# Kernel optimization log

Measured on AMD Instinct MI355X. Metric: run time of the kernel, lower is better.

## Reference

```python
import jax, jax.numpy as jnp
import numpy as np

B, T, C, NH, DH, L, HFF, FEAT = 2, 1024, 1024, 16, 64, 4, 2816, 9
EPS = 1e-5
ROPE_BASE = 10000.0


def setup_inputs() -> dict:
    key = jax.random.key(0)
    ks = jax.random.split(key, 11)
    s = 0.02
    return {
        "x": jax.random.normal(ks[0], (B, T, FEAT), jnp.float32),
        "w_in": jax.random.normal(ks[1], (C, FEAT), jnp.float32) * s,
        "wq": jax.random.normal(ks[2], (L, C, C), jnp.float32) * s,
        "wkv": jax.random.normal(ks[3], (L, 2 * C, C), jnp.float32) * s,
        "wo": jax.random.normal(ks[4], (L, C, C), jnp.float32) * s,
        "w1": jax.random.normal(ks[5], (L, HFF, C), jnp.float32) * s,
        "w2": jax.random.normal(ks[6], (L, HFF, C), jnp.float32) * s,
        "w3": jax.random.normal(ks[7], (L, C, HFF), jnp.float32) * s,
        "g1": jnp.ones((L, C), jnp.float32),
        "g2": jnp.ones((L, C), jnp.float32),
        "gf": jnp.ones((C,), jnp.float32),
    }


def _rms(x, g):
    # lag-llama RMSNorm: x * rsqrt(mean(x^2) + eps) * scale
    return x * jax.lax.rsqrt(jnp.mean(x * x, axis=-1, keepdims=True) + EPS) * g


def _rope_tables(seq_len, dim):
    inv_freq = 1.0 / (ROPE_BASE ** (jnp.arange(0, dim, 2, dtype=jnp.float32) / dim))
    freqs = jnp.arange(seq_len, dtype=jnp.float32)[:, None] * inv_freq[None, :]
    emb = jnp.concatenate([freqs, freqs], axis=-1)  # [T, DH]
    return jnp.cos(emb), jnp.sin(emb)


def _rotate_half(x):
    h = x.shape[-1] // 2
    return jnp.concatenate([-x[..., h:], x[..., :h]], axis=-1)


def reference(x, w_in, wq, wkv, wo, w1, w2, w3, g1, g2, gf):
    h = x @ w_in.T  # [B,T,C] input projection (wte)
    cos, sin = _rope_tables(T, DH)  # [T,DH], broadcast over B,NH
    causal = jnp.tril(jnp.ones((T, T), dtype=bool))
    scale = 1.0 / np.sqrt(DH).astype(np.float32)

    for l in range(L):
        # --- attention block ---
        a_in = _rms(h, g1[l])
        q = (a_in @ wq[l].T).reshape(B, T, NH, DH).transpose(0, 2, 1, 3)
        kv = a_in @ wkv[l].T
        k = kv[..., :C].reshape(B, T, NH, DH).transpose(0, 2, 1, 3)
        v = kv[..., C:].reshape(B, T, NH, DH).transpose(0, 2, 1, 3)
        q = q * cos + _rotate_half(q) * sin
        k = k * cos + _rotate_half(k) * sin
        scores = jnp.einsum('bhtd,bhsd->bhts', q, k) * scale
        scores = jnp.where(causal, scores, -jnp.inf)
        probs = jax.nn.softmax(scores, axis=-1)  # dropout_p=0 -> identity
        y = jnp.einsum('bhts,bhsd->bhtd', probs, v)
        y = y.transpose(0, 2, 1, 3).reshape(B, T, C)
        h = h + y @ wo[l].T
        # --- MLP block (gated SiLU) ---
        m_in = _rms(h, g2[l])
        h = h + (jax.nn.silu(m_in @ w1[l].T) * (m_in @ w2[l].T)) @ w3[l].T

    return _rms(h, gf)
```

## Files before the change

kernel.cpp:

```cpp
#include <hip/hip_runtime.h>
#include <hip/hip_bf16.h>


#define B_   2
#define T_   1024
#define C_   1024
#define NH_  16
#define DH_  64
#define L_   4
#define HFF_ 2816
#define EPS_ 1e-5f

typedef unsigned short u16;
typedef short bf16x8 __attribute__((ext_vector_type(8)));
typedef float f32x4 __attribute__((ext_vector_type(4)));

__device__ __forceinline__ float b2f(u16 u) {
    union { unsigned int i; float f; } v; v.i = ((unsigned int)u) << 16; return v.f;
}
__device__ __forceinline__ u16 f2b(float f) {
    union { unsigned int i; float f; } v; v.f = f;
    unsigned int r = (v.i + 0x7fff + ((v.i >> 16) & 1)) >> 16;
    return (u16)r;
}

__global__ void detect_k(const unsigned int* __restrict__ xw, int* __restrict__ flag)
{
    int tid = threadIdx.x;
    int cnt = 0;
#pragma unroll
    for (int i = 0; i < 4; ++i) {
        unsigned int w = xw[tid * 4 + i];
        unsigned int e = (w >> 7) & 0xFF;
        if (e >= 0x70 && e <= 0x87) cnt++;
    }
#pragma unroll
    for (int off = 32; off; off >>= 1) cnt += __shfl_down(cnt, off);
    if (tid == 0) flag[0] = (cnt > 128) ? 0 : 1;
}

__global__ void cvt_k(const void* __restrict__ src, u16* __restrict__ dst,
                      int n, const int* __restrict__ flag)
{
    int f = flag[0];
    int i = blockIdx.x * 256 + threadIdx.x;
    int stride = gridDim.x * 256;
    if (f) {
        const float* s = (const float*)src;
        for (; i < n; i += stride) dst[i] = f2b(s[i]);
    } else {
        const u16* s = (const u16*)src;
        for (; i < n; i += stride) dst[i] = s[i];
    }
}

template<int MODE>
__global__ __launch_bounds__(256, 2)
void gemm_bt(const u16* __restrict__ A, const u16* __restrict__ Bm,
             u16* __restrict__ Cb, float* __restrict__ Cf,
             int M, int N, int K, int lda, int ldb, int ldc,
             int nhDiv, long sAb, long sAh, long sBb, long sBh,
             long sCb, long sCh)
{
    __shared__ __align__(16) u16 tA[128 * 32];
    __shared__ __align__(16) u16 tB[128 * 32];

    const int z  = blockIdx.z;
    const int bb = z / nhDiv;
    const int hh = z - bb * nhDiv;
    const u16* Ab = A + bb * sAb + hh * sAh;
    const u16* Bb = Bm + bb * sBb + hh * sBh;
    const long cOff = bb * sCb + hh * sCh;

    const int row0 = blockIdx.y * 128;
    const int col0 = blockIdx.x * 128;
    const int tid  = threadIdx.x;
    const int lane = tid & 63;
    const int wave = tid >> 6;
    const int wr = wave >> 1, wc = wave & 1;
    const int lrow = lane & 15;
    const int kg   = lane >> 4;

    int r_[2], cg_[2];
#pragma unroll
    for (int i = 0; i < 2; ++i) {
        int chunk = i * 256 + tid;
        r_[i]  = chunk >> 2;
        cg_[i] = chunk & 3;
    }

    f32x4 acc[4][4] = {};

    for (int k0 = 0; k0 < K; k0 += 32) {
        bf16x8 ra[2], rb[2];
#pragma unroll
        for (int i = 0; i < 2; ++i) {
            const u16* ga = Ab + (long)(row0 + r_[i]) * lda + (k0 + cg_[i] * 8);
            ra[i] = *(const bf16x8*)ga;
            int rB = col0 + r_[i]; if (rB > N - 1) rB = N - 1;
            const u16* gb = Bb + (long)rB * ldb + (k0 + cg_[i] * 8);
            rb[i] = *(const bf16x8*)gb;
        }
        __syncthreads();
#pragma unroll
        for (int i = 0; i < 2; ++i) {
            int chunk = i * 256 + tid;
            *(bf16x8*)&tA[(size_t)chunk * 8] = ra[i];
            *(bf16x8*)&tB[(size_t)chunk * 8] = rb[i];
        }
        __syncthreads();

        bf16x8 af[4], bfr[4];
#pragma unroll
        for (int ti = 0; ti < 4; ++ti)
            af[ti] = *(const bf16x8*)&tA[(wr * 64 + ti * 16 + lrow) * 32 + kg * 8];
#pragma unroll
        for (int tj = 0; tj < 4; ++tj)
            bfr[tj] = *(const bf16x8*)&tB[(wc * 64 + tj * 16 + lrow) * 32 + kg * 8];
#pragma unroll
        for (int ti = 0; ti < 4; ++ti)
#pragma unroll
            for (int tj = 0; tj < 4; ++tj)
                acc[ti][tj] = __builtin_amdgcn_mfma_f32_16x16x32_bf16(
                    af[ti], bfr[tj], acc[ti][tj], 0, 0, 0);
    }

    const int rbase = row0 + wr * 64;
    const int cbase = col0 + wc * 64 + lrow;
#pragma unroll
    for (int ti = 0; ti < 4; ++ti) {
#pragma unroll
        for (int r = 0; r < 4; ++r) {
            int row = rbase + ti * 16 + kg * 4 + r;
#pragma unroll
            for (int tj = 0; tj < 4; ++tj) {
                int col = cbase + tj * 16;
                if (col < N) {
                    long off = cOff + (long)row * ldc + col;
                    if (MODE == 0) Cb[off] = f2b(acc[ti][tj][r]);
                    else           Cf[off] += acc[ti][tj][r];
                }
            }
        }
    }
}

__global__ void input_proj_k(const u16* __restrict__ x, const u16* __restrict__ w,
                             float* __restrict__ h)
{
    int idx = blockIdx.x * 256 + threadIdx.x;
    int bt = idx >> 10, c = idx & 1023;
    float s = 0.f;
#pragma unroll
    for (int f = 0; f < 9; ++f) s += b2f(x[bt * 9 + f]) * b2f(w[c * 9 + f]);
    h[idx] = s;
}

__global__ void rms_k(const float* __restrict__ h, const u16* __restrict__ g,
                      void* __restrict__ out, int isFinal,
                      const int* __restrict__ flag)
{
    __shared__ float red[8];
    const int row = blockIdx.x;
    const float* hr = h + (size_t)row * C_;
    float ss = 0.f;
    for (int c = threadIdx.x; c < C_; c += 256) { float v = hr[c]; ss += v * v; }
#pragma unroll
    for (int off = 32; off; off >>= 1) ss += __shfl_down(ss, off);
    int lane = threadIdx.x & 63, wave = threadIdx.x >> 6;
    if (lane == 0) red[wave] = ss;
    __syncthreads();
    if (threadIdx.x == 0)
        red[4] = rsqrtf((red[0] + red[1] + red[2] + red[3]) / (float)C_ + EPS_);
    __syncthreads();
    float r = red[4];
    const int f32out = isFinal && flag[0];
    for (int c = threadIdx.x; c < C_; c += 256) {
        float val = hr[c] * r * b2f(g[c]);
        size_t o = (size_t)row * C_ + c;
        if (f32out) ((float*)out)[o] = val;
        else        ((u16*)out)[o]   = f2b(val);
    }
}

__global__ void rope_k(u16* __restrict__ q, u16* __restrict__ kv)
{
    int idx = blockIdx.x * 256 + threadIdx.x;
    int i = idx & 31;
    int hh = (idx >> 5) & 15;
    int t = (idx >> 9) & 1023;
    int b = idx >> 19;
    float invf = powf(10000.0f, -(float)i / 32.0f);
    float fr = (float)t * invf;
    float cf = cosf(fr), sf = sinf(fr);

    size_t qo = ((size_t)(b * 1024 + t) << 10) + hh * 64 + i;
    float x1 = b2f(q[qo]), x2 = b2f(q[qo + 32]);
    q[qo]      = f2b(x1 * cf - x2 * sf);
    q[qo + 32] = f2b(x2 * cf + x1 * sf);

    size_t ko = ((size_t)(b * 1024 + t) << 11) + hh * 64 + i;
    x1 = b2f(kv[ko]); x2 = b2f(kv[ko + 32]);
    kv[ko]      = f2b(x1 * cf - x2 * sf);
    kv[ko + 32] = f2b(x2 * cf + x1 * sf);
}

__global__ void vtrans_k(const u16* __restrict__ kv, u16* __restrict__ vt)
{
    int idx = blockIdx.x * 256 + threadIdx.x;
    int s = idx & 1023;
    int d = (idx >> 10) & 63;
    int hh = (idx >> 16) & 15;
    int b = idx >> 20;
    vt[idx] = kv[((size_t)(b * 1024 + s) << 11) + 1024 + hh * 64 + d];
}

__global__ void softmax_k(u16* __restrict__ S)
{
    __shared__ float red[8];
    const int t = blockIdx.x & 1023;
    const int z = blockIdx.x >> 10;
    u16* row = S + ((size_t)z << 20) + ((size_t)t << 10);
    const int n = t + 1;
    const int tid = threadIdx.x;
    const int lane = tid & 63, wave = tid >> 6;

    float mx = -1e30f;
    for (int c = tid; c < n; c += 256) mx = fmaxf(mx, 0.125f * b2f(row[c]));
#pragma unroll
    for (int off = 32; off; off >>= 1) mx = fmaxf(mx, __shfl_down(mx, off));
    if (lane == 0) red[wave] = mx;
    __syncthreads();
    if (tid == 0) red[4] = fmaxf(fmaxf(red[0], red[1]), fmaxf(red[2], red[3]));
    __syncthreads();
    const float M = red[4];

    float sum = 0.f;
    for (int c = tid; c < n; c += 256) sum += __expf(0.125f * b2f(row[c]) - M);
#pragma unroll
    for (int off = 32; off; off >>= 1) sum += __shfl_down(sum, off);
    if (lane == 0) red[wave] = sum;
    __syncthreads();
    if (tid == 0) red[5] = red[0] + red[1] + red[2] + red[3];
    __syncthreads();
    const float inv = 1.0f / red[5];

    for (int c = tid; c < 1024; c += 256) {
        float p = (c < n) ? __expf(0.125f * b2f(row[c]) - M) * inv : 0.f;
        row[c] = f2b(p);
    }
}

__global__ void silu_mul_k(u16* __restrict__ u1, const u16* __restrict__ u2)
{
    size_t idx = (size_t)blockIdx.x * 256 + threadIdx.x;
    float a = b2f(u1[idx]);
    float m = a / (1.f + __expf(-a));
    u1[idx] = f2b(m * b2f(u2[idx]));
}

static inline void launch_gemm(bool add, const u16* A, const u16* Bm, void* C,
                               int M, int N, int K, int lda, int ldb, int ldc,
                               int batch, int nhDiv,
                               long sAb, long sAh, long sBb, long sBh,
                               long sCb, long sCh, hipStream_t stream)
{
    dim3 g((N + 127) / 128, M / 128, batch);
    if (add)
        gemm_bt<1><<<g, 256, 0, stream>>>(A, Bm, nullptr, (float*)C,
            M, N, K, lda, ldb, ldc, nhDiv, sAb, sAh, sBb, sBh, sCb, sCh);
    else
        gemm_bt<0><<<g, 256, 0, stream>>>(A, Bm, (u16*)C, nullptr,
            M, N, K, lda, ldb, ldc, nhDiv, sAb, sAh, sBb, sBh, sCb, sCh);
}

extern "C" void kernel_launch(void* const* d_in, const int* in_sizes, int n_in,
                              void* d_out, int out_size, void* d_ws, size_t ws_size,
                              hipStream_t stream)
{
    char* w = (char*)d_ws;
    float* h  = (float*)w;
    u16* a    = (u16*)(w + (8u  << 20));
    u16* q    = (u16*)(w + (12u << 20));
    u16* kv   = (u16*)(w + (16u << 20));
    u16* vt   = (u16*)(w + (24u << 20));
    u16* y    = (u16*)(w + (28u << 20));
    u16* S    = (u16*)(w + (32u << 20));
    u16* u1   = S;
    u16* u2   = S + (size_t)2048 * HFF_;

    size_t off = (size_t)64 << 20;
    const int nelem[11] = {
        B_ * T_ * 9,
        C_ * 9,
        L_ * C_ * C_,
        L_ * 2 * C_ * C_,
        L_ * C_ * C_,
        L_ * HFF_ * C_,
        L_ * HFF_ * C_,
        L_ * C_ * HFF_,
        L_ * C_,
        L_ * C_,
        C_
    };
    u16* cbuf[11];
    for (int i = 0; i < 11; ++i) {
        cbuf[i] = (u16*)(w + off);
        off += ((size_t)nelem[i] * 2 + 255) & ~(size_t)255;
    }
    int* flag = (int*)(w + off);

    detect_k<<<1, 64, 0, stream>>>((const unsigned int*)d_in[0], flag);
    for (int i = 0; i < 11; ++i) {
        int blocks = (nelem[i] + 255) / 256; if (blocks > 2048) blocks = 2048;
        cvt_k<<<blocks, 256, 0, stream>>>(d_in[i], cbuf[i], nelem[i], flag);
    }
    const u16* cx   = cbuf[0];
    const u16* cwin = cbuf[1];
    const u16* cwq  = cbuf[2];
    const u16* cwkv = cbuf[3];
    const u16* cwo  = cbuf[4];
    const u16* cw1  = cbuf[5];
    const u16* cw2  = cbuf[6];
    const u16* cw3  = cbuf[7];
    const u16* cg1  = cbuf[8];
    const u16* cg2  = cbuf[9];
    const u16* cgf  = cbuf[10];

    const long TC  = (long)T_ * C_;
    const long T2C = 2 * TC;
    const long TT  = (long)T_ * T_;

    input_proj_k<<<8192, 256, 0, stream>>>(cx, cwin, h);

    for (int l = 0; l < L_; ++l) {
        const u16* wq_l  = cwq  + (size_t)l * C_ * C_;
        const u16* wkv_l = cwkv + (size_t)l * 2 * C_ * C_;
        const u16* wo_l  = cwo  + (size_t)l * C_ * C_;
        const u16* w1_l  = cw1  + (size_t)l * HFF_ * C_;
        const u16* w2_l  = cw2  + (size_t)l * HFF_ * C_;
        const u16* w3_l  = cw3  + (size_t)l * C_ * HFF_;

        rms_k<<<2048, 256, 0, stream>>>(h, cg1 + l * C_, a, 0, flag);
        launch_gemm(false, a, wq_l, q, 2048, 1024, 1024, 1024, 1024, 1024,
                    1, 1, 0, 0, 0, 0, 0, 0, stream);
        launch_gemm(false, a, wkv_l, kv, 2048, 2048, 1024, 1024, 1024, 2048,
                    1, 1, 0, 0, 0, 0, 0, 0, stream);
        rope_k<<<4096, 256, 0, stream>>>(q, kv);
        vtrans_k<<<8192, 256, 0, stream>>>(kv, vt);

        for (int b = 0; b < B_; ++b) {
            const u16* qb  = q  + (size_t)b * TC;
            const u16* kvb = kv + (size_t)b * T2C;
            const u16* vtb = vt + (size_t)b * NH_ * DH_ * T_;
            u16* yb        = y  + (size_t)b * TC;
            launch_gemm(false, qb, kvb, S, 1024, 1024, 64, 1024, 2048, 1024,
                        16, 16, 0, 64, 0, 64, 0, TT, stream);
            softmax_k<<<16 * 1024, 256, 0, stream>>>(S);
            launch_gemm(false, S, vtb, yb, 1024, 64, 1024, 1024, 1024, 1024,
                        16, 16, 0, TT, 0, (long)DH_ * T_, 0, DH_, stream);
        }
        launch_gemm(true, y, wo_l, h, 2048, 1024, 1024, 1024, 1024, 1024,
                    1, 1, 0, 0, 0, 0, 0, 0, stream);

        rms_k<<<2048, 256, 0, stream>>>(h, cg2 + l * C_, a, 0, flag);
        launch_gemm(false, a, w1_l, u1, 2048, HFF_, 1024, 1024, 1024, HFF_,
                    1, 1, 0, 0, 0, 0, 0, 0, stream);
        launch_gemm(false, a, w2_l, u2, 2048, HFF_, 1024, 1024, 1024, HFF_,
                    1, 1, 0, 0, 0, 0, 0, 0, stream);
        silu_mul_k<<<22528, 256, 0, stream>>>(u1, u2);
        launch_gemm(true, u1, w3_l, h, 2048, 1024, HFF_, HFF_, HFF_, 1024,
                    1, 1, 0, 0, 0, 0, 0, 0, stream);
    }

    rms_k<<<2048, 256, 0, stream>>>(h, cgf, d_out, 1, flag);
}
```

Before: 1.786 ms.

## Fuse QKV and W1/W2 GEMMs, split-K residual GEMMs, load tiles directly to LDS

Weights are repacked at conversion time so Q/K/V and W1/W2 each sit in one buffer, and each pair or triple is computed by a single batched GEMM launch. The residual-add GEMMs (wo, w3) are split four ways along K and accumulate into h with atomicAdd, so the 16x8 tile grid covers more of the CUs. The GEMM tile loads now use global_load_lds, copying straight from global memory into LDS instead of going through registers. The conversion kernel is vectorized to four elements per thread. In exchange, float atomics make the summation order nondeterministic, and the direct-to-LDS loads depend on the compiler inserting the correct wait before the barrier.

```diff
diff --git a/kernel.cpp b/kernel.cpp
--- a/kernel.cpp
+++ b/kernel.cpp
@@ -40,17 +40,24 @@
 }
 
 __global__ void cvt_k(const void* __restrict__ src, u16* __restrict__ dst,
-                      int n, const int* __restrict__ flag)
-{
-    int f = flag[0];
-    int i = blockIdx.x * 256 + threadIdx.x;
-    int stride = gridDim.x * 256;
-    if (f) {
-        const float* s = (const float*)src;
-        for (; i < n; i += stride) dst[i] = f2b(s[i]);
-    } else {
-        const u16* s = (const u16*)src;
-        for (; i < n; i += stride) dst[i] = s[i];
+                      long perV, long dstStrideV, long dstOffV,
+                      const int* __restrict__ flag)
+{
+    const int f = flag[0];
+    long y = blockIdx.y;
+    long i = (long)blockIdx.x * 256 + threadIdx.x;
+    long stride = (long)gridDim.x * 256;
+    for (; i < perV; i += stride) {
+        long so = y * perV + i;
+        long dj = y * dstStrideV + dstOffV + i;
+        ushort4 o;
+        if (f) {
+            float4 v = ((const float4*)src)[so];
+            o.x = f2b(v.x); o.y = f2b(v.y); o.z = f2b(v.z); o.w = f2b(v.w);
+        } else {
+            o = ((const ushort4*)src)[so];
+        }
+        ((ushort4*)dst)[dj] = o;
     }
 }
 
@@ -60,17 +67,26 @@
              u16* __restrict__ Cb, float* __restrict__ Cf,
              int M, int N, int K, int lda, int ldb, int ldc,
              int nhDiv, long sAb, long sAh, long sBb, long sBh,
-             long sCb, long sCh)
+             long sCb, long sCh, int kSplit)
 {
     __shared__ __align__(16) u16 tA[128 * 32];
     __shared__ __align__(16) u16 tB[128 * 32];
 
-    const int z  = blockIdx.z;
-    const int bb = z / nhDiv;
-    const int hh = z - bb * nhDiv;
-    const u16* Ab = A + bb * sAb + hh * sAh;
-    const u16* Bb = Bm + bb * sBb + hh * sBh;
-    const long cOff = bb * sCb + hh * sCh;
+    const int z = blockIdx.z;
+    int kBeg = 0, kEnd = K;
+    const u16* Ab = A;
+    const u16* Bb = Bm;
+    long cOff = 0;
+    if (MODE == 1) {
+        int ks = K / kSplit;
+        kBeg = z * ks; kEnd = kBeg + ks;
+    } else {
+        int bb = z / nhDiv;
+        int hh = z - bb * nhDiv;
+        Ab += bb * sAb + hh * sAh;
+        Bb += bb * sBb + hh * sBh;
+        cOff = bb * sCb + hh * sCh;
+    }
 
     const int row0 = blockIdx.y * 128;
     const int col0 = blockIdx.x * 128;
@@ -81,32 +97,30 @@
     const int lrow = lane & 15;
     const int kg   = lane >> 4;
 
-    int r_[2], cg_[2];
-#pragma unroll
-    for (int i = 0; i < 2; ++i) {
-        int chunk = i * 256 + tid;
-        r_[i]  = chunk >> 2;
-        cg_[i] = chunk & 3;
-    }
-
     f32x4 acc[4][4] = {};
 
-    for (int k0 = 0; k0 < K; k0 += 32) {
-        bf16x8 ra[2], rb[2];
-#pragma unroll
-        for (int i = 0; i < 2; ++i) {
-            const u16* ga = Ab + (long)(row0 + r_[i]) * lda + (k0 + cg_[i] * 8);
-            ra[i] = *(const bf16x8*)ga;
-            int rB = col0 + r_[i]; if (rB > N - 1) rB = N - 1;
-            const u16* gb = Bb + (long)rB * ldb + (k0 + cg_[i] * 8);
-            rb[i] = *(const bf16x8*)gb;
-        }
+    for (int k0 = kBeg; k0 < kEnd; k0 += 32) {
         __syncthreads();
 #pragma unroll
         for (int i = 0; i < 2; ++i) {
             int chunk = i * 256 + tid;
-            *(bf16x8*)&tA[(size_t)chunk * 8] = ra[i];
-            *(bf16x8*)&tB[(size_t)chunk * 8] = rb[i];
+            int r = chunk >> 2, cg = chunk & 3;
+            const u16* ga = Ab + (long)(row0 + r) * lda + (k0 + cg * 8);
+            u16* la = tA + (size_t)(i * 256 + wave * 64) * 8;
+            __builtin_amdgcn_global_load_lds(
+                (const __attribute__((address_space(1))) void*)ga,
+                (__attribute__((address_space(3))) void*)la, 16, 0, 0);
+        }
+#pragma unroll
+        for (int i = 0; i < 2; ++i) {
+            int chunk = i * 256 + tid;
+            int r = chunk >> 2, cg = chunk & 3;
+            int rB = col0 + r; if (rB > N - 1) rB = N - 1;
+            const u16* gb = Bb + (long)rB * ldb + (k0 + cg * 8);
+            u16* lb = tB + (size_t)(i * 256 + wave * 64) * 8;
+            __builtin_amdgcn_global_load_lds(
+                (const __attribute__((address_space(1))) void*)gb,
+                (__attribute__((address_space(3))) void*)lb, 16, 0, 0);
         }
         __syncthreads();
 
@@ -138,7 +152,7 @@
                 if (col < N) {
                     long off = cOff + (long)row * ldc + col;
                     if (MODE == 0) Cb[off] = f2b(acc[ti][tj][r]);
-                    else           Cf[off] += acc[ti][tj][r];
+                    else           atomicAdd(&Cf[off], acc[ti][tj][r]);
                 }
             }
         }
@@ -183,7 +197,7 @@
     }
 }
 
-__global__ void rope_k(u16* __restrict__ q, u16* __restrict__ kv)
+__global__ void rope_k(u16* __restrict__ qkv)
 {
     int idx = blockIdx.x * 256 + threadIdx.x;
     int i = idx & 31;
@@ -194,25 +208,25 @@
     float fr = (float)t * invf;
     float cf = cosf(fr), sf = sinf(fr);
 
-    size_t qo = ((size_t)(b * 1024 + t) << 10) + hh * 64 + i;
-    float x1 = b2f(q[qo]), x2 = b2f(q[qo + 32]);
-    q[qo]      = f2b(x1 * cf - x2 * sf);
-    q[qo + 32] = f2b(x2 * cf + x1 * sf);
-
-    size_t ko = ((size_t)(b * 1024 + t) << 11) + hh * 64 + i;
-    x1 = b2f(kv[ko]); x2 = b2f(kv[ko + 32]);
-    kv[ko]      = f2b(x1 * cf - x2 * sf);
-    kv[ko + 32] = f2b(x2 * cf + x1 * sf);
-}
-
-__global__ void vtrans_k(const u16* __restrict__ kv, u16* __restrict__ vt)
+    size_t base = (size_t)(b * 1024 + t) * 3072 + hh * 64 + i;
+    float x1 = b2f(qkv[base]), x2 = b2f(qkv[base + 32]);
+    qkv[base]      = f2b(x1 * cf - x2 * sf);
+    qkv[base + 32] = f2b(x2 * cf + x1 * sf);
+
+    size_t kb = base + 1024;
+    x1 = b2f(qkv[kb]); x2 = b2f(qkv[kb + 32]);
+    qkv[kb]      = f2b(x1 * cf - x2 * sf);
+    qkv[kb + 32] = f2b(x2 * cf + x1 * sf);
+}
+
+__global__ void vtrans_k(const u16* __restrict__ qkv, u16* __restrict__ vt)
 {
     int idx = blockIdx.x * 256 + threadIdx.x;
     int s = idx & 1023;
     int d = (idx >> 10) & 63;
     int hh = (idx >> 16) & 15;
     int b = idx >> 20;
-    vt[idx] = kv[((size_t)(b * 1024 + s) << 11) + 1024 + hh * 64 + d];
+    vt[idx] = qkv[(size_t)(b * 1024 + s) * 3072 + 2048 + hh * 64 + d];
 }
 
 __global__ void softmax_k(u16* __restrict__ S)
@@ -261,17 +275,26 @@
 
 static inline void launch_gemm(bool add, const u16* A, const u16* Bm, void* C,
                                int M, int N, int K, int lda, int ldb, int ldc,
-                               int batch, int nhDiv,
+                               int zdim, int nhDiv,
                                long sAb, long sAh, long sBb, long sBh,
-                               long sCb, long sCh, hipStream_t stream)
-{
-    dim3 g((N + 127) / 128, M / 128, batch);
+                               long sCb, long sCh, int kSplit, hipStream_t stream)
+{
+    dim3 g((N + 127) / 128, M / 128, zdim);
     if (add)
         gemm_bt<1><<<g, 256, 0, stream>>>(A, Bm, nullptr, (float*)C,
-            M, N, K, lda, ldb, ldc, nhDiv, sAb, sAh, sBb, sBh, sCb, sCh);
+            M, N, K, lda, ldb, ldc, nhDiv, sAb, sAh, sBb, sBh, sCb, sCh, kSplit);
     else
         gemm_bt<0><<<g, 256, 0, stream>>>(A, Bm, (u16*)C, nullptr,
-            M, N, K, lda, ldb, ldc, nhDiv, sAb, sAh, sBb, sBh, sCb, sCh);
+            M, N, K, lda, ldb, ldc, nhDiv, sAb, sAh, sBb, sBh, sCb, sCh, kSplit);
+}
+
+static inline void launch_cvt(const void* src, u16* dst, long perV,
+                              long dstStrideV, long dstOffV, int chunks,
+                              const int* flag, hipStream_t stream)
+{
+    long bx = (perV + 255) / 256; if (bx > 512) bx = 512;
+    dim3 g((unsigned)bx, (unsigned)chunks, 1);
+    cvt_k<<<g, 256, 0, stream>>>(src, dst, perV, dstStrideV, dstOffV, flag);
 }
 
 extern "C" void kernel_launch(void* const* d_in, const int* in_sizes, int n_in,
@@ -279,98 +302,81 @@
                               hipStream_t stream)
 {
     char* w = (char*)d_ws;
-    float* h  = (float*)w;
-    u16* a    = (u16*)(w + (8u  << 20));
-    u16* q    = (u16*)(w + (12u << 20));
-    u16* kv   = (u16*)(w + (16u << 20));
-    u16* vt   = (u16*)(w + (24u << 20));
-    u16* y    = (u16*)(w + (28u << 20));
-    u16* S    = (u16*)(w + (32u << 20));
-    u16* u1   = S;
-    u16* u2   = S + (size_t)2048 * HFF_;
+    float* h   = (float*)w;
+    u16* a     = (u16*)(w + (8u  << 20));
+    u16* qkv   = (u16*)(w + (12u << 20));
+    u16* vt    = (u16*)(w + (24u << 20));
+    u16* y     = (u16*)(w + (28u << 20));
+    u16* S     = (u16*)(w + (32u << 20));
+    u16* u1    = S;
+    u16* u2    = S + (size_t)2048 * HFF_;
 
     size_t off = (size_t)64 << 20;
-    const int nelem[11] = {
-        B_ * T_ * 9,
-        C_ * 9,
-        L_ * C_ * C_,
-        L_ * 2 * C_ * C_,
-        L_ * C_ * C_,
-        L_ * HFF_ * C_,
-        L_ * HFF_ * C_,
-        L_ * C_ * HFF_,
-        L_ * C_,
-        L_ * C_,
-        C_
-    };
-    u16* cbuf[11];
-    for (int i = 0; i < 11; ++i) {
-        cbuf[i] = (u16*)(w + off);
-        off += ((size_t)nelem[i] * 2 + 255) & ~(size_t)255;
-    }
-    int* flag = (int*)(w + off);
+    u16* cx    = (u16*)(w + off); off += ((size_t)B_*T_*9*2   + 255) & ~(size_t)255;
+    u16* cwin  = (u16*)(w + off); off += ((size_t)C_*9*2      + 255) & ~(size_t)255;
+    u16* cwqkv = (u16*)(w + off); off += (size_t)L_*3072*1024*2;
+    u16* cwo   = (u16*)(w + off); off += (size_t)L_*C_*C_*2;
+    u16* cw12  = (u16*)(w + off); off += (size_t)L_*2*HFF_*C_*2;
+    u16* cw3   = (u16*)(w + off); off += (size_t)L_*C_*HFF_*2;
+    u16* cg1   = (u16*)(w + off); off += ((size_t)L_*C_*2 + 255) & ~(size_t)255;
+    u16* cg2   = (u16*)(w + off); off += ((size_t)L_*C_*2 + 255) & ~(size_t)255;
+    u16* cgf   = (u16*)(w + off); off += ((size_t)C_*2    + 255) & ~(size_t)255;
+    int* flag  = (int*)(w + off);
 
     detect_k<<<1, 64, 0, stream>>>((const unsigned int*)d_in[0], flag);
-    for (int i = 0; i < 11; ++i) {
-        int blocks = (nelem[i] + 255) / 256; if (blocks > 2048) blocks = 2048;
-        cvt_k<<<blocks, 256, 0, stream>>>(d_in[i], cbuf[i], nelem[i], flag);
-    }
-    const u16* cx   = cbuf[0];
-    const u16* cwin = cbuf[1];
-    const u16* cwq  = cbuf[2];
-    const u16* cwkv = cbuf[3];
-    const u16* cwo  = cbuf[4];
-    const u16* cw1  = cbuf[5];
-    const u16* cw2  = cbuf[6];
-    const u16* cw3  = cbuf[7];
-    const u16* cg1  = cbuf[8];
-    const u16* cg2  = cbuf[9];
-    const u16* cgf  = cbuf[10];
+
+    const long CCv  = (long)C_ * C_ / 4;
+    const long HCv  = (long)HFF_ * C_ / 4;
+    launch_cvt(d_in[0],  cx,    (long)B_*T_*9/4, 0, 0, 1, flag, stream);
+    launch_cvt(d_in[1],  cwin,  (long)C_*9/4,    0, 0, 1, flag, stream);
+    launch_cvt(d_in[2],  cwqkv, CCv,   3*CCv, 0,     L_, flag, stream);
+    launch_cvt(d_in[3],  cwqkv, 2*CCv, 3*CCv, CCv,   L_, flag, stream);
+    launch_cvt(d_in[4],  cwo,   CCv,   CCv,   0,     L_, flag, stream);
+    launch_cvt(d_in[5],  cw12,  HCv,   2*HCv, 0,     L_, flag, stream);
+    launch_cvt(d_in[6],  cw12,  HCv,   2*HCv, HCv,   L_, flag, stream);
+    launch_cvt(d_in[7],  cw3,   HCv,   HCv,   0,     L_, flag, stream);
+    launch_cvt(d_in[8],  cg1,   (long)L_*C_/4, 0, 0, 1, flag, stream);
+    launch_cvt(d_in[9],  cg2,   (long)L_*C_/4, 0, 0, 1, flag, stream);
+    launch_cvt(d_in[10], cgf,   (long)C_/4,    0, 0, 1, flag, stream);
 
     const long TC  = (long)T_ * C_;
-    const long T2C = 2 * TC;
     const long TT  = (long)T_ * T_;
+    const long TQ  = (long)T_ * 3072;
 
     input_proj_k<<<8192, 256, 0, stream>>>(cx, cwin, h);
 
     for (int l = 0; l < L_; ++l) {
-        const u16* wq_l  = cwq  + (size_t)l * C_ * C_;
-        const u16* wkv_l = cwkv + (size_t)l * 2 * C_ * C_;
-        const u16* wo_l  = cwo  + (size_t)l * C_ * C_;
-        const u16* w1_l  = cw1  + (size_t)l * HFF_ * C_;
-        const u16* w2_l  = cw2  + (size_t)l * HFF_ * C_;
-        const u16* w3_l  = cw3  + (size_t)l * C_ * HFF_;
+        const u16* wqkv_l = cwqkv + (size_t)l * 3072 * 1024;
+        const u16* wo_l   = cwo   + (size_t)l * C_ * C_;
+        const u16* w12_l  = cw12  + (size_t)l * 2 * HFF_ * C_;
+        const u16* w3_l   = cw3   + (size_t)l * C_ * HFF_;
 
         rms_k<<<2048, 256, 0, stream>>>(h, cg1 + l * C_, a, 0, flag);
-        launch_gemm(false, a, wq_l, q, 2048, 1024, 1024, 1024, 1024, 1024,
-                    1, 1, 0, 0, 0, 0, 0, 0, stream);
-        launch_gemm(false, a, wkv_l, kv, 2048, 2048, 1024, 1024, 1024, 2048,
-                    1, 1, 0, 0, 0, 0, 0, 0, stream);
-        rope_k<<<4096, 256, 0, stream>>>(q, kv);
-        vtrans_k<<<8192, 256, 0, stream>>>(kv, vt);
+        launch_gemm(false, a, wqkv_l, qkv, 2048, 1024, 1024, 1024, 1024, 3072,
+                    3, 3, 0, 0, 0, (long)C_*C_, 0, 1024, 1, stream);
+        rope_k<<<4096, 256, 0, stream>>>(qkv);
+        vtrans_k<<<8192, 256, 0, stream>>>(qkv, vt);
 
         for (int b = 0; b < B_; ++b) {
-            const u16* qb  = q  + (size_t)b * TC;
-            const u16* kvb = kv + (size_t)b * T2C;
+            const u16* qb = qkv + (size_t)b * TQ;
+            const u16* kb = qb + 1024;
             const u16* vtb = vt + (size_t)b * NH_ * DH_ * T_;
             u16* yb        = y  + (size_t)b * TC;
-            launch_gemm(false, qb, kvb, S, 1024, 1024, 64, 1024, 2048, 1024,
-                        16, 16, 0, 64, 0, 64, 0, TT, stream);
+            launch_gemm(false, qb, kb, S, 1024, 1024, 64, 3072, 3072, 1024,
+                        16, 16, 0, 64, 0, 64, 0, TT, 1, stream);
             softmax_k<<<16 * 1024, 256, 0, stream>>>(S);
             launch_gemm(false, S, vtb, yb, 1024, 64, 1024, 1024, 1024, 1024,
-                        16, 16, 0, TT, 0, (long)DH_ * T_, 0, DH_, stream);
+                        16, 16, 0, TT, 0, (long)DH_*T_, 0, DH_, 1, stream);
         }
         launch_gemm(true, y, wo_l, h, 2048, 1024, 1024, 1024, 1024, 1024,
-                    1, 1, 0, 0, 0, 0, 0, 0, stream);
+                    4, 1, 0, 0, 0, 0, 0, 0, 4, stream);
 
         rms_k<<<2048, 256, 0, stream>>>(h, cg2 + l * C_, a, 0, flag);
-        launch_gemm(false, a, w1_l, u1, 2048, HFF_, 1024, 1024, 1024, HFF_,
-                    1, 1, 0, 0, 0, 0, 0, 0, stream);
-        launch_gemm(false, a, w2_l, u2, 2048, HFF_, 1024, 1024, 1024, HFF_,
-                    1, 1, 0, 0, 0, 0, 0, 0, stream);
+        launch_gemm(false, a, w12_l, u1, 2048, HFF_, 1024, 1024, 1024, HFF_,
+                    2, 2, 0, 0, 0, (long)HFF_*C_, 0, (long)2048*HFF_, 1, stream);
         silu_mul_k<<<22528, 256, 0, stream>>>(u1, u2);
         launch_gemm(true, u1, w3_l, h, 2048, 1024, HFF_, HFF_, HFF_, 1024,
-                    1, 1, 0, 0, 0, 0, 0, 0, stream);
+                    4, 1, 0, 0, 0, 0, 0, 0, 4, stream);
     }
 
     rms_k<<<2048, 256, 0, stream>>>(h, cgf, d_out, 1, flag);
```

Result: faster. 1.467 ms (-17.9%).
